# Kernel optimization log

Hardware: AMD Instinct MI355X
Metric: run time of the kernel (lower is better)

## Reference

```python
import jax, jax.numpy as jnp
import numpy as np

EPS = 1e-6

def setup_inputs() -> dict:
    key = jax.random.key(0)
    k = jax.random.split(key, 7)
    N, E, d_i, d_o = 50000, 800000, 128, 128
    x = jax.random.normal(k[0], (N, d_i), dtype=jnp.float32)
    src = jax.random.randint(k[1], (E,), 0, N)
    tgt = jax.random.randint(k[2], (E,), 0, N)
    # xavier_uniform for both linear weights (torch nn.init.xavier_uniform_)
    lim_f = float(np.sqrt(6.0 / (2 * d_i + d_o)))
    Wf = jax.random.uniform(k[3], (d_o, 2 * d_i), jnp.float32, -lim_f, lim_f)
    lim_w = float(np.sqrt(6.0 / (2 * d_i + 1)))
    Ww = jax.random.uniform(k[4], (1, 2 * d_i), jnp.float32, -lim_w, lim_w)
    # torch Linear default bias init: U(-1/sqrt(fan_in), 1/sqrt(fan_in))
    lb = float(1.0 / np.sqrt(2 * d_i))
    bf = jax.random.uniform(k[5], (d_o,), jnp.float32, -lb, lb)
    bw = jax.random.uniform(k[6], (1,), jnp.float32, -lb, lb)
    return {"x": x, "Wf": Wf, "bf": bf, "Ww": Ww, "bw": bw,
            "src": src, "tgt": tgt, "num_nodes": N}


def reference(x, Wf, bf, Ww, bw, src, tgt, num_nodes):
    # gather endpoints and build edge features [E, 2*d_i]
    h = jnp.concatenate([x[src], x[tgt]], axis=1)
    # fused linear + relu message: [E, d_o]
    y = jax.nn.relu(h @ Wf.T + bf)
    # unnormalized attention score per edge: [E, 1]
    a = h @ Ww.T + bw
    # scatter-sum over target nodes (equivalent to mm(Mtgt, .))
    a_sum = jax.ops.segment_sum(a, tgt, num_segments=num_nodes) + EPS
    o = jax.ops.segment_sum(y * a, tgt, num_segments=num_nodes) / a_sum
    return o
```

## Files before the change

kernel.cpp:

```cpp
#include <hip/hip_runtime.h>


typedef short bf16x8 __attribute__((ext_vector_type(8)));
typedef short bf16x4 __attribute__((ext_vector_type(4)));
typedef float f32x4  __attribute__((ext_vector_type(4)));

__device__ inline short f32_to_bf16_rne(float f) {
    unsigned u = __float_as_uint(f);
    unsigned r = u + 0x7fffu + ((u >> 16) & 1u);
    return (short)(r >> 16);
}
__device__ inline float bf16s_to_f32(short s) {
    return __uint_as_float(((unsigned)(unsigned short)s) << 16);
}

__global__ __launch_bounds__(256) void k_wconv(
    const float* __restrict__ Wf, short* __restrict__ whp, short* __restrict__ wlp)
{
    int tid = blockIdx.x * 256 + threadIdx.x;
    if (tid >= 4096) return;
    int ct = tid >> 8, kt = (tid >> 6) & 3, lane = tid & 63;
    int c = ct * 16 + (lane & 15);
    int kbase = kt * 32 + (lane >> 4) * 8;
    bf16x8 h, l;
    #pragma unroll
    for (int j = 0; j < 8; ++j) {
        int k = kbase + j;
        float v = (c < 128) ? Wf[c * 256 + k] : Wf[(c - 128) * 256 + 128 + k];
        short hs = f32_to_bf16_rne(v);
        h[j] = hs;
        l[j] = f32_to_bf16_rne(v - bf16s_to_f32(hs));
    }
    *(bf16x8*)(whp + (size_t)tid * 8) = h;
    *(bf16x8*)(wlp + (size_t)tid * 8) = l;
}

__global__ __launch_bounds__(256) void k_transform(
    const float* __restrict__ x, const short* __restrict__ whp,
    const short* __restrict__ wlp, const float* __restrict__ bf,
    const float* __restrict__ Ww, const float* __restrict__ bw,
    short* __restrict__ Ub, float* __restrict__ Vb,
    double* __restrict__ p, double* __restrict__ q, int N)
{
    __shared__ __attribute__((aligned(16))) char smem[32768];
    const int t = threadIdx.x, wv = t >> 6, lane = t & 63;
    const int n0 = blockIdx.x * 64;

    #pragma unroll
    for (int r = 0; r < 8; ++r) {
        int idx = r * 1024 + t * 4;
        int row = idx >> 7, col = idx & 127;
        int n = n0 + row;
        const float* sp = x + (size_t)((n < N) ? n : (N - 1)) * 128 + col;
        f32x4 v = *(const f32x4*)sp;
        bf16x4 hh, ll;
        #pragma unroll
        for (int j = 0; j < 4; ++j) {
            short hs = f32_to_bf16_rne(v[j]);
            hh[j] = hs;
            ll[j] = f32_to_bf16_rne(v[j] - bf16s_to_f32(hs));
        }
        int ba = (row * 256 + col * 2) ^ ((row & 7) << 4);
        *(bf16x4*)(smem + ba)         = hh;
        *(bf16x4*)(smem + 16384 + ba) = ll;
    }

    {
        int row = wv * 16 + (lane >> 2);
        int n = n0 + row;
        int c0 = (lane & 3) * 32;
        const float* xr = x + (size_t)((n < N) ? n : (N - 1)) * 128 + c0;
        double ps = 0.0, qs = 0.0;
        #pragma unroll
        for (int jj = 0; jj < 32; jj += 4) {
            f32x4 v = *(const f32x4*)(xr + jj);
            #pragma unroll
            for (int j = 0; j < 4; ++j) {
                ps += (double)v[j] * (double)Ww[c0 + jj + j];
                qs += (double)v[j] * (double)Ww[128 + c0 + jj + j];
            }
        }
        ps += __shfl_xor(ps, 1); ps += __shfl_xor(ps, 2);
        qs += __shfl_xor(qs, 1); qs += __shfl_xor(qs, 2);
        if ((lane & 3) == 0 && n < N) {
            p[n] = ps;
            q[n] = qs + (double)bw[0];
        }
    }
    __syncthreads();

    f32x4 acc[4][4] = {};
    #pragma unroll
    for (int tt = 0; tt < 4; ++tt) {
        const int ct = wv * 4 + tt;
        bf16x8 Wh[4], Wl[4];
        #pragma unroll
        for (int kt = 0; kt < 4; ++kt) {
            size_t off = (size_t)((ct * 4 + kt) * 64 + lane) * 8;
            Wh[kt] = *(const bf16x8*)(whp + off);
            Wl[kt] = *(const bf16x8*)(wlp + off);
        }
        #pragma unroll
        for (int kt = 0; kt < 4; ++kt) {
            #pragma unroll
            for (int ns = 0; ns < 4; ++ns) {
                int row = ns * 16 + (lane & 15);
                int ba = (row * 256 + kt * 64 + (lane >> 4) * 16) ^ ((row & 7) << 4);
                bf16x8 xhf = *(const bf16x8*)(smem + ba);
                bf16x8 xlf = *(const bf16x8*)(smem + 16384 + ba);
                acc[tt][ns] = __builtin_amdgcn_mfma_f32_16x16x32_bf16(Wh[kt], xhf, acc[tt][ns], 0, 0, 0);
                acc[tt][ns] = __builtin_amdgcn_mfma_f32_16x16x32_bf16(Wh[kt], xlf, acc[tt][ns], 0, 0, 0);
                acc[tt][ns] = __builtin_amdgcn_mfma_f32_16x16x32_bf16(Wl[kt], xhf, acc[tt][ns], 0, 0, 0);
            }
        }
    }
    __syncthreads();

    if (wv < 2) {
        #pragma unroll
        for (int tt = 0; tt < 4; ++tt) {
            int cb = (wv * 4 + tt) * 64 + (lane >> 4) * 16;
            #pragma unroll
            for (int ns = 0; ns < 4; ++ns) {
                int node = ns * 16 + (lane & 15);
                int ba = (node * 512 + cb) ^ ((node & 7) << 4);
                *(f32x4*)(smem + ba) = acc[tt][ns];
            }
        }
    }
    __syncthreads();
    #pragma unroll
    for (int r = 0; r < 8; ++r) {
        int fo = r * 4096 + t * 16;
        int row = fo >> 9;
        int col = (fo & 511) >> 2;
        if (n0 + row < N) {
            f32x4 v = *(const f32x4*)(smem + (fo ^ ((row & 7) << 4)));
            bf16x4 b;
            b[0] = f32_to_bf16_rne(v[0]); b[1] = f32_to_bf16_rne(v[1]);
            b[2] = f32_to_bf16_rne(v[2]); b[3] = f32_to_bf16_rne(v[3]);
            *(bf16x4*)(Ub + (size_t)(n0 + row) * 128 + col) = b;
        }
    }
    __syncthreads();

    if (wv >= 2) {
        #pragma unroll
        for (int tt = 0; tt < 4; ++tt) {
            int cb = ((wv - 2) * 4 + tt) * 64 + (lane >> 4) * 16;
            #pragma unroll
            for (int ns = 0; ns < 4; ++ns) {
                int node = ns * 16 + (lane & 15);
                int ba = (node * 512 + cb) ^ ((node & 7) << 4);
                *(f32x4*)(smem + ba) = acc[tt][ns];
            }
        }
    }
    __syncthreads();
    #pragma unroll
    for (int r = 0; r < 8; ++r) {
        int fo = r * 4096 + t * 16;
        int row = fo >> 9;
        int col = (fo & 511) >> 2;
        if (n0 + row < N) {
            f32x4 v = *(const f32x4*)(smem + (fo ^ ((row & 7) << 4)));
            f32x4 bias = *(const f32x4*)(bf + col);
            v[0] += bias[0]; v[1] += bias[1]; v[2] += bias[2]; v[3] += bias[3];
            *(f32x4*)(Vb + (size_t)(n0 + row) * 128 + col) = v;
        }
    }
}


__global__ __launch_bounds__(256) void k_hist(
    const int* __restrict__ tgt, int* __restrict__ counts, int E)
{
    int e = blockIdx.x * 256 + threadIdx.x;
    if (e < E) atomicAdd(&counts[tgt[e]], 1);
}

__global__ __launch_bounds__(256) void k_scan1(
    const int* __restrict__ counts, int* __restrict__ incl,
    int* __restrict__ partials, int N)
{
    __shared__ int sh[256];
    int t = threadIdx.x;
    int i = blockIdx.x * 256 + t;
    int v = (i < N) ? counts[i] : 0;
    sh[t] = v;
    __syncthreads();
    #pragma unroll
    for (int off = 1; off < 256; off <<= 1) {
        int add = (t >= off) ? sh[t - off] : 0;
        __syncthreads();
        sh[t] += add;
        __syncthreads();
    }
    if (i < N) incl[i] = sh[t];
    if (t == 255) partials[blockIdx.x] = sh[255];
}

__global__ __launch_bounds__(256) void k_scan2(int* __restrict__ partials, int nb)
{
    __shared__ int sh[256];
    int t = threadIdx.x;
    int v = (t < nb) ? partials[t] : 0;
    sh[t] = v;
    __syncthreads();
    #pragma unroll
    for (int off = 1; off < 256; off <<= 1) {
        int add = (t >= off) ? sh[t - off] : 0;
        __syncthreads();
        sh[t] += add;
        __syncthreads();
    }
    if (t < nb) partials[t] = sh[t] - v;
}

__global__ __launch_bounds__(256) void k_scan3(
    const int* __restrict__ counts, const int* __restrict__ incl,
    const int* __restrict__ partials, int* __restrict__ offsets,
    int* __restrict__ cursor, int N)
{
    int i = blockIdx.x * 256 + threadIdx.x;
    if (i >= N) return;
    int off = incl[i] - counts[i] + partials[i >> 8];
    offsets[i] = off;
    cursor[i]  = off;
}

__global__ __launch_bounds__(256) void k_scatter(
    const int* __restrict__ src, const int* __restrict__ tgt,
    int* __restrict__ cursor, int* __restrict__ srcs,
    int E, int wsz, int nchunk)
{
    const int win  = blockIdx.x & 7;
    const int step = gridDim.x >> 3;
    for (int c = blockIdx.x >> 3; c < nchunk; c += step) {
        int e = c * 256 + threadIdx.x;
        if (e < E) {
            int tg = tgt[e];
            if (tg / wsz == win) {
                int pos = atomicAdd(&cursor[tg], 1);
                srcs[pos] = src[e];
            }
        }
    }
}


__global__ __launch_bounds__(256) void k_node(
    const short* __restrict__ Ub, const float* __restrict__ Vb,
    const double* __restrict__ p, const double* __restrict__ q,
    const int* __restrict__ offsets, const int* __restrict__ counts,
    const int* __restrict__ srcs, float* __restrict__ out, int N)
{
    int idx  = blockIdx.x * 256 + threadIdx.x;
    int n    = idx >> 5;
    int lane = threadIdx.x & 31;
    if (n >= N) return;

    float4 Vn = ((const float4*)(Vb + (size_t)n * 128))[lane];
    double qn = q[n];
    int beg = offsets[n];
    int cnt = counts[n];

    float ax = 0.f, ay = 0.f, az = 0.f, aw = 0.f;
    double asum = 0.0;

    int i = 0;
    for (; i + 4 <= cnt; i += 4) {
        int s0 = srcs[beg + i + 0];
        int s1 = srcs[beg + i + 1];
        int s2 = srcs[beg + i + 2];
        int s3 = srcs[beg + i + 3];
        bf16x4 u0 = *(const bf16x4*)(Ub + (size_t)s0 * 128 + lane * 4);
        bf16x4 u1 = *(const bf16x4*)(Ub + (size_t)s1 * 128 + lane * 4);
        bf16x4 u2 = *(const bf16x4*)(Ub + (size_t)s2 * 128 + lane * 4);
        bf16x4 u3 = *(const bf16x4*)(Ub + (size_t)s3 * 128 + lane * 4);
        double a0 = p[s0] + qn, a1 = p[s1] + qn, a2 = p[s2] + qn, a3 = p[s3] + qn;
        float f0 = (float)a0, f1 = (float)a1, f2 = (float)a2, f3 = (float)a3;

        ax += fmaxf(bf16s_to_f32(u0[0]) + Vn.x, 0.f) * f0;
        ay += fmaxf(bf16s_to_f32(u0[1]) + Vn.y, 0.f) * f0;
        az += fmaxf(bf16s_to_f32(u0[2]) + Vn.z, 0.f) * f0;
        aw += fmaxf(bf16s_to_f32(u0[3]) + Vn.w, 0.f) * f0;
        asum += a0;
        ax += fmaxf(bf16s_to_f32(u1[0]) + Vn.x, 0.f) * f1;
        ay += fmaxf(bf16s_to_f32(u1[1]) + Vn.y, 0.f) * f1;
        az += fmaxf(bf16s_to_f32(u1[2]) + Vn.z, 0.f) * f1;
        aw += fmaxf(bf16s_to_f32(u1[3]) + Vn.w, 0.f) * f1;
        asum += a1;
        ax += fmaxf(bf16s_to_f32(u2[0]) + Vn.x, 0.f) * f2;
        ay += fmaxf(bf16s_to_f32(u2[1]) + Vn.y, 0.f) * f2;
        az += fmaxf(bf16s_to_f32(u2[2]) + Vn.z, 0.f) * f2;
        aw += fmaxf(bf16s_to_f32(u2[3]) + Vn.w, 0.f) * f2;
        asum += a2;
        ax += fmaxf(bf16s_to_f32(u3[0]) + Vn.x, 0.f) * f3;
        ay += fmaxf(bf16s_to_f32(u3[1]) + Vn.y, 0.f) * f3;
        az += fmaxf(bf16s_to_f32(u3[2]) + Vn.z, 0.f) * f3;
        aw += fmaxf(bf16s_to_f32(u3[3]) + Vn.w, 0.f) * f3;
        asum += a3;
    }
    for (; i < cnt; ++i) {
        int s = srcs[beg + i];
        bf16x4 u = *(const bf16x4*)(Ub + (size_t)s * 128 + lane * 4);
        double a = p[s] + qn;
        float af = (float)a;
        ax += fmaxf(bf16s_to_f32(u[0]) + Vn.x, 0.f) * af;
        ay += fmaxf(bf16s_to_f32(u[1]) + Vn.y, 0.f) * af;
        az += fmaxf(bf16s_to_f32(u[2]) + Vn.z, 0.f) * af;
        aw += fmaxf(bf16s_to_f32(u[3]) + Vn.w, 0.f) * af;
        asum += a;
    }

    double inv = 1.0 / (asum + 1e-6);
    float4 o;
    o.x = (float)((double)ax * inv);
    o.y = (float)((double)ay * inv);
    o.z = (float)((double)az * inv);
    o.w = (float)((double)aw * inv);
    ((float4*)(out + (size_t)n * 128))[lane] = o;
}

extern "C" void kernel_launch(void* const* d_in, const int* in_sizes, int n_in,
                              void* d_out, int out_size, void* d_ws, size_t ws_size,
                              hipStream_t stream)
{
    const float* x   = (const float*)d_in[0];
    const float* Wf  = (const float*)d_in[1];
    const float* bf  = (const float*)d_in[2];
    const float* Ww  = (const float*)d_in[3];
    const float* bw  = (const float*)d_in[4];
    const int*   src = (const int*)d_in[5];
    const int*   tgt = (const int*)d_in[6];

    const int N = in_sizes[0] / 128;
    const int E = in_sizes[5];
    float* out = (float*)d_out;

    char* w = (char*)d_ws;
    short*  Ub       = (short*)w;                 w += (size_t)N * 128 * sizeof(short);
    float*  Vb       = (float*)w;                 w += (size_t)N * 128 * sizeof(float);
    double* p        = (double*)w;                w += (size_t)N * sizeof(double);
    double* q        = (double*)w;                w += (size_t)N * sizeof(double);
    int*    counts   = (int*)w;                   w += (size_t)N * sizeof(int);
    int*    incl     = (int*)w;                   w += (size_t)N * sizeof(int);
    int*    offsets  = (int*)w;                   w += (size_t)N * sizeof(int);
    int*    cursor   = (int*)w;                   w += (size_t)N * sizeof(int);
    int*    partials = (int*)w;                   w += 4096;
    int*    srcs     = (int*)w;                   w += (size_t)E * sizeof(int);
    short*  whp      = (short*)w;                 w += 256 * 128 * sizeof(short);
    short*  wlp      = (short*)w;

    hipMemsetAsync(counts, 0, (size_t)N * sizeof(int), stream);

    k_wconv<<<16, 256, 0, stream>>>(Wf, whp, wlp);
    k_transform<<<(N + 63) / 64, 256, 0, stream>>>(
        x, whp, wlp, bf, Ww, bw, Ub, Vb, p, q, N);

    int ebk = (E + 255) / 256;
    int nbk = (N + 255) / 256;
    k_hist<<<ebk, 256, 0, stream>>>(tgt, counts, E);
    k_scan1<<<nbk, 256, 0, stream>>>(counts, incl, partials, N);
    k_scan2<<<1, 256, 0, stream>>>(partials, nbk);
    k_scan3<<<nbk, 256, 0, stream>>>(counts, incl, partials, offsets, cursor, N);

    int wsz = (N + 7) / 8;
    k_scatter<<<4096, 256, 0, stream>>>(src, tgt, cursor, srcs, E, wsz, ebk);

    long long nthreads = (long long)N * 32;
    k_node<<<(int)((nthreads + 255) / 256), 256, 0, stream>>>(
        Ub, Vb, p, q, offsets, counts, srcs, out, N);
}
```

Before: 238.2 us.

## Replace three-kernel scan with single-block scan and windowed histogram

The three-pass prefix sum (block scan, partials scan, fixup) becomes one 1024-thread single-block kernel. It uses wave shuffles and carries a running total across 4096-element chunks, which removes two launches and the intermediate incl/partials arrays. The histogram kernel now uses the same XCD-windowed grid as the scatter kernel, so atomics on each target range stay in one die's cache. The cost is a serial single-block scan over 50k nodes, and the histogram reads tgt eight times across windows.

After: 249.6 us. 4.8% more time.

```diff
diff --git a/kernel.cpp b/kernel.cpp
--- a/kernel.cpp
+++ b/kernel.cpp
@@ -173,60 +173,64 @@
 
 
 __global__ __launch_bounds__(256) void k_hist(
-    const int* __restrict__ tgt, int* __restrict__ counts, int E)
-{
-    int e = blockIdx.x * 256 + threadIdx.x;
-    if (e < E) atomicAdd(&counts[tgt[e]], 1);
-}
-
-__global__ __launch_bounds__(256) void k_scan1(
-    const int* __restrict__ counts, int* __restrict__ incl,
-    int* __restrict__ partials, int N)
-{
-    __shared__ int sh[256];
-    int t = threadIdx.x;
-    int i = blockIdx.x * 256 + t;
-    int v = (i < N) ? counts[i] : 0;
-    sh[t] = v;
-    __syncthreads();
-    #pragma unroll
-    for (int off = 1; off < 256; off <<= 1) {
-        int add = (t >= off) ? sh[t - off] : 0;
+    const int* __restrict__ tgt, int* __restrict__ counts,
+    int E, int wsz, int nchunk)
+{
+    const int win  = blockIdx.x & 7;
+    const int step = gridDim.x >> 3;
+    for (int c = blockIdx.x >> 3; c < nchunk; c += step) {
+        int e = c * 256 + threadIdx.x;
+        if (e < E) {
+            int tg = tgt[e];
+            if (tg / wsz == win) atomicAdd(&counts[tg], 1);
+        }
+    }
+}
+
+__global__ __launch_bounds__(1024) void k_scan(
+    const int* __restrict__ counts, int* __restrict__ offsets,
+    int* __restrict__ cursor, int N)
+{
+    __shared__ int wsums[16];
+    __shared__ int carrySh;
+    const int t = threadIdx.x, lane = t & 63, wv = t >> 6;
+    if (t == 0) carrySh = 0;
+    __syncthreads();
+    for (int base = 0; base < N; base += 4096) {
+        int i0 = base + t * 4;
+        int4 v = make_int4(0, 0, 0, 0);
+        if (i0 + 3 < N) v = *(const int4*)(counts + i0);
+        else {
+            if (i0 + 0 < N) v.x = counts[i0 + 0];
+            if (i0 + 1 < N) v.y = counts[i0 + 1];
+            if (i0 + 2 < N) v.z = counts[i0 + 2];
+        }
+        int tsum = ((v.x + v.y) + (v.z + v.w));
+        int s = tsum;
+        #pragma unroll
+        for (int off = 1; off < 64; off <<= 1) {
+            int u = __shfl_up(s, off, 64);
+            if (lane >= off) s += u;
+        }
+        if (lane == 63) wsums[wv] = s;
         __syncthreads();
-        sh[t] += add;
+        int wpre = 0;
+        #pragma unroll
+        for (int k = 0; k < 15; ++k) if (k < wv) wpre += wsums[k];
+        int excl = carrySh + wpre + (s - tsum);
+        int o0 = excl, o1 = o0 + v.x, o2 = o1 + v.y, o3 = o2 + v.z;
+        if (i0 + 3 < N) {
+            *(int4*)(offsets + i0) = make_int4(o0, o1, o2, o3);
+            *(int4*)(cursor  + i0) = make_int4(o0, o1, o2, o3);
+        } else {
+            if (i0 + 0 < N) { offsets[i0 + 0] = o0; cursor[i0 + 0] = o0; }
+            if (i0 + 1 < N) { offsets[i0 + 1] = o1; cursor[i0 + 1] = o1; }
+            if (i0 + 2 < N) { offsets[i0 + 2] = o2; cursor[i0 + 2] = o2; }
+        }
         __syncthreads();
-    }
-    if (i < N) incl[i] = sh[t];
-    if (t == 255) partials[blockIdx.x] = sh[255];
-}
-
-__global__ __launch_bounds__(256) void k_scan2(int* __restrict__ partials, int nb)
-{
-    __shared__ int sh[256];
-    int t = threadIdx.x;
-    int v = (t < nb) ? partials[t] : 0;
-    sh[t] = v;
-    __syncthreads();
-    #pragma unroll
-    for (int off = 1; off < 256; off <<= 1) {
-        int add = (t >= off) ? sh[t - off] : 0;
+        if (t == 1023) carrySh += wpre + s;
         __syncthreads();
-        sh[t] += add;
-        __syncthreads();
-    }
-    if (t < nb) partials[t] = sh[t] - v;
-}
-
-__global__ __launch_bounds__(256) void k_scan3(
-    const int* __restrict__ counts, const int* __restrict__ incl,
-    const int* __restrict__ partials, int* __restrict__ offsets,
-    int* __restrict__ cursor, int N)
-{
-    int i = blockIdx.x * 256 + threadIdx.x;
-    if (i >= N) return;
-    int off = incl[i] - counts[i] + partials[i >> 8];
-    offsets[i] = off;
-    cursor[i]  = off;
+    }
 }
 
 __global__ __launch_bounds__(256) void k_scatter(
@@ -345,10 +349,8 @@
     double* p        = (double*)w;                w += (size_t)N * sizeof(double);
     double* q        = (double*)w;                w += (size_t)N * sizeof(double);
     int*    counts   = (int*)w;                   w += (size_t)N * sizeof(int);
-    int*    incl     = (int*)w;                   w += (size_t)N * sizeof(int);
     int*    offsets  = (int*)w;                   w += (size_t)N * sizeof(int);
     int*    cursor   = (int*)w;                   w += (size_t)N * sizeof(int);
-    int*    partials = (int*)w;                   w += 4096;
     int*    srcs     = (int*)w;                   w += (size_t)E * sizeof(int);
     short*  whp      = (short*)w;                 w += 256 * 128 * sizeof(short);
     short*  wlp      = (short*)w;
@@ -360,13 +362,9 @@
         x, whp, wlp, bf, Ww, bw, Ub, Vb, p, q, N);
 
     int ebk = (E + 255) / 256;
-    int nbk = (N + 255) / 256;
-    k_hist<<<ebk, 256, 0, stream>>>(tgt, counts, E);
-    k_scan1<<<nbk, 256, 0, stream>>>(counts, incl, partials, N);
-    k_scan2<<<1, 256, 0, stream>>>(partials, nbk);
-    k_scan3<<<nbk, 256, 0, stream>>>(counts, incl, partials, offsets, cursor, N);
-
     int wsz = (N + 7) / 8;
+    k_hist<<<4096, 256, 0, stream>>>(tgt, counts, E, wsz, ebk);
+    k_scan<<<1, 1024, 0, stream>>>(counts, offsets, cursor, N);
     k_scatter<<<4096, 256, 0, stream>>>(src, tgt, cursor, srcs, E, wsz, ebk);
 
     long long nthreads = (long long)N * 32;
```
